# Performance work log

Measured on AMD Instinct MI355X. Metric: run time of the kernel, lower is better.

## Reference

```python
import jax, jax.numpy as jnp
import numpy as np

IN_CH = 512
SCALES = (128.0, 256.0, 512.0)
ASPECT_RATIOS = (0.5, 1.0, 2.0)
NUM_ANCHORS = 9
PRE_NMS_TOPK = 10000
POST_NMS_TOPK = 2000
NMS_THRESH = 0.7


def conv2d(x, w, b, pad):
    y = jax.lax.conv_general_dilated(
        x, w, window_strides=(1, 1), padding=[(pad, pad), (pad, pad)],
        dimension_numbers=('NCHW', 'OIHW', 'NCHW'))
    return y + b[None, :, None, None]


def generate_anchors(image_hw, feat_hw, dtype=jnp.float32):
    img_h, img_w = image_hw
    gh, gw = feat_hw
    stride_h = img_h // gh
    stride_w = img_w // gw
    scale = jnp.asarray(SCALES, dtype)
    ar = jnp.asarray(ASPECT_RATIOS, dtype)
    h_ratio = jnp.sqrt(ar)
    w_ratio = 1.0 / h_ratio
    ws = (w_ratio[:, None] * scale[None, :]).reshape(-1)  # (9,) ratio-major
    hs = (h_ratio[:, None] * scale[None, :]).reshape(-1)
    base = jnp.round(jnp.stack([-ws, -hs, ws, hs], axis=1) / 2.0)  # (9,4)
    shift_x = jnp.arange(gw, dtype=dtype) * stride_w
    shift_y = jnp.arange(gh, dtype=dtype) * stride_h
    sy, sx = jnp.meshgrid(shift_y, shift_x, indexing='ij')
    sx = sx.reshape(-1)
    sy = sy.reshape(-1)
    shifts = jnp.stack([sx, sy, sx, sy], axis=1)  # (gh*gw, 4)
    anchors = (shifts[:, None, :] + base[None, :, :]).reshape(-1, 4)
    return anchors


def decode_boxes(deltas, anchors):
    # deltas: (N,4) [dx,dy,dw,dh]; anchors: (N,4) [x1,y1,x2,y2]
    w = anchors[:, 2] - anchors[:, 0]
    h = anchors[:, 3] - anchors[:, 1]
    cx = anchors[:, 0] + 0.5 * w
    cy = anchors[:, 1] + 0.5 * h
    dx, dy, dw, dh = deltas[:, 0], deltas[:, 1], deltas[:, 2], deltas[:, 3]
    pcx = w * dx + cx
    pcy = h * dy + cy
    pw = jnp.exp(dw) * w
    ph = jnp.exp(dh) * h
    return jnp.stack([pcx - 0.5 * pw, pcy - 0.5 * ph,
                      pcx + 0.5 * pw, pcy + 0.5 * ph], axis=1)


def clamp_boxes(b, image_hw):
    h, w = image_hw
    return jnp.stack([jnp.clip(b[:, 0], 0.0, w), jnp.clip(b[:, 1], 0.0, h),
                      jnp.clip(b[:, 2], 0.0, w), jnp.clip(b[:, 3], 0.0, h)], axis=1)


def pairwise_iou(boxes1, boxes2):
    area1 = (boxes1[:, 2] - boxes1[:, 0]) * (boxes1[:, 3] - boxes1[:, 1])
    area2 = (boxes2[:, 2] - boxes2[:, 0]) * (boxes2[:, 3] - boxes2[:, 1])
    xl = jnp.maximum(boxes1[:, None, 0], boxes2[None, :, 0])
    yt = jnp.maximum(boxes1[:, None, 1], boxes2[None, :, 1])
    xr = jnp.minimum(boxes1[:, None, 2], boxes2[None, :, 2])
    yb = jnp.minimum(boxes1[:, None, 3], boxes2[None, :, 3])
    inter = jnp.clip(xr - xl, 0.0) * jnp.clip(yb - yt, 0.0)
    return inter / (area1[:, None] + area2[None, :] - inter)


def nms_keep(boxes_sorted, thresh):
    # boxes already sorted by score descending; returns bool keep mask
    n = boxes_sorted.shape[0]
    iou = pairwise_iou(boxes_sorted, boxes_sorted)  # (n,n) ~ the memory-bound hot spot
    idx = jnp.arange(n)
    def body(i, keep):
        suppressed = jnp.any((iou[i] > thresh) & keep & (idx < i))
        return keep.at[i].set(jnp.logical_not(suppressed))
    return jax.lax.fori_loop(0, n, body, jnp.ones((n,), dtype=bool))


def filter_proposals(proposals, logits, image_hw):
    scores = jax.nn.sigmoid(logits.reshape(-1))
    top_scores, top_idx = jax.lax.top_k(scores, PRE_NMS_TOPK)  # sorted descending
    props = proposals[top_idx]
    props = clamp_boxes(props, image_hw)
    keep = nms_keep(jax.lax.stop_gradient(props), NMS_THRESH)
    masked = jnp.where(keep, jax.lax.stop_gradient(top_scores), -1.0)
    sel_scores, sel = jax.lax.top_k(masked, POST_NMS_TOPK)
    valid = sel_scores >= 0.0  # sigmoid scores are >0; padded slots are -1
    out_boxes = jnp.where(valid[:, None], props[sel], 0.0)
    out_scores = jnp.where(valid, top_scores[sel], 0.0)
    return out_boxes, out_scores


def setup_inputs() -> dict:
    key = jax.random.key(0)
    ks = jax.random.split(key, 6)
    image = jax.random.normal(ks[0], (1, 3, 800, 800), jnp.float32)
    feat = jax.random.normal(ks[1], (1, IN_CH, 50, 50), jnp.float32)
    # small init scales keep exp(dw) numerically tame (mimics real conv init)
    rpn_w = jax.random.normal(ks[2], (IN_CH, IN_CH, 3, 3), jnp.float32) * 0.02
    rpn_b = jnp.zeros((IN_CH,), jnp.float32)
    cls_w = jax.random.normal(ks[3], (NUM_ANCHORS, IN_CH, 1, 1), jnp.float32) * 0.01
    cls_b = jnp.zeros((NUM_ANCHORS,), jnp.float32)
    box_w = jax.random.normal(ks[4], (NUM_ANCHORS * 4, IN_CH, 1, 1), jnp.float32) * 0.01
    box_b = jnp.zeros((NUM_ANCHORS * 4,), jnp.float32)
    return {"image": image, "feat": feat, "rpn_w": rpn_w, "rpn_b": rpn_b,
            "cls_w": cls_w, "cls_b": cls_b, "box_w": box_w, "box_b": box_b}


def reference(image, feat, rpn_w, rpn_b, cls_w, cls_b, box_w, box_b):
    B, _, H, W = feat.shape  # B == 1 as in the original (single-image RPN)
    rpn_feat = jax.nn.relu(conv2d(feat, rpn_w, rpn_b, pad=1))
    cls = conv2d(rpn_feat, cls_w, cls_b, pad=0)        # (1, 9, H, W)
    box = conv2d(rpn_feat, box_w, box_b, pad=0)        # (1, 36, H, W)
    anchors = generate_anchors(image.shape[-2:], (H, W), feat.dtype)  # (H*W*9, 4)
    # cls: NCHW -> NHWC -> (N_anchors, 1), anchor order = (y, x, anchor)
    cls_flat = jnp.transpose(cls, (0, 2, 3, 1)).reshape(-1, 1)
    # box: (1,9,4,H,W) -> (1,H,W,9,4) -> (N_anchors, 4)
    deltas = jnp.transpose(box.reshape(B, NUM_ANCHORS, 4, H, W), (0, 3, 4, 1, 2)).reshape(-1, 4)
    proposals = decode_boxes(deltas, anchors)
    props, scores = filter_proposals(proposals, jax.lax.stop_gradient(cls_flat), image.shape[-2:])
    return props, scores, cls_flat
```

## Files before the change

### kernel.cpp

```cpp
#include <hip/hip_runtime.h>
#include <cstdint>
#include <cstddef>


typedef unsigned long long ull;
typedef double d4 __attribute__((ext_vector_type(4)));

#define NANCH 9
#define NPIX  2500
#define CIN   512
#define COUT  512
#define KTOT  4608
#define KSEG  2304
#define NBOX  22500
#define TOPK1 10000
#define TOPK2 2000
#define WORDS 157
#define NHEAD 45
#define HPAD  48

__global__ __launch_bounds__(256) void wtrans(const float* __restrict__ w,
                                              float* __restrict__ wT) {
  __shared__ float t[36][65];
  const int ci0 = blockIdx.x * 4;
  const int co0 = blockIdx.y * 64;
  const int tid = threadIdx.x;
  const int co_l = tid >> 2, cq = tid & 3;
  const float* src = w + (size_t)(co0 + co_l) * KTOT + (ci0 + cq) * 9;
#pragma unroll
  for (int r = 0; r < 9; ++r) t[r * 4 + cq][co_l] = src[r];
  __syncthreads();
  const int co_w = tid & 63, rw0 = tid >> 6;
#pragma unroll
  for (int m = 0; m < 9; ++m) {
    int rw = rw0 + 4 * m;
    int tap = rw >> 2, cqq = rw & 3;
    wT[((size_t)tap * 512 + ci0 + cqq) * 512 + co0 + co_w] = t[rw][co_w];
  }
}

__global__ __launch_bounds__(256, 5) void conv_gemm(const float* __restrict__ feat,
                                                    const float* __restrict__ wT,
                                                    double* __restrict__ part) {
  const int p0  = blockIdx.x * 32;
  const int co0 = blockIdx.y * 64;
  const int z   = blockIdx.z;
  const int kseg0 = z * KSEG;
  __shared__ float As[2][32][40];
  __shared__ float Bs[2][32][72];
  const int tid  = threadIdx.x;
  const int lane = tid & 63;
  const int wave = tid >> 6;
  const int quad = lane >> 4;
  const int l16  = lane & 15;
  const int wp = (wave & 1) * 16;
  const int wc = (wave >> 1) * 32;
  const int plA = tid & 31, kAr = tid >> 5;
  const int pB = p0 + plA;
  const int py = pB / 50, px = pB - py * 50;
  const int coB = tid & 63, kBr = tid >> 6;

  int pmap[4];
  {
    double av_p = (quad == 0) ? (double)(l16 + 1) : (quad == 1 ? 1.0 : 0.0);
    double bv_p = (quad == 0) ? 1.0 : (quad == 1 ? (double)(1000 * (l16 + 1)) : 0.0);
    d4 dp = (d4){0.0, 0.0, 0.0, 0.0};
    dp = __builtin_amdgcn_mfma_f64_16x16x4f64(av_p, bv_p, dp, 0, 0, 0);
#pragma unroll
    for (int r = 0; r < 4; ++r) {
      int iv = (int)(dp[r] + 0.5);
      int mm = iv % 1000 - 1;
      int nn = iv / 1000 - 1;
      pmap[r] = (mm & 255) | (nn << 8);
    }
  }

  d4 acc[2];
#pragma unroll
  for (int i = 0; i < 2; ++i) acc[i] = (d4){0.0, 0.0, 0.0, 0.0};

  const int NCH = KSEG / 32;

  float fa[4], fb[8];

  auto loadA = [&](int cc) {
    int kk0 = kseg0 + cc * 32;
    int tap = kk0 >> 9;
    int ci0 = kk0 & 511;
    int ky = (tap * 11) >> 5;
    int kx = tap - 3 * ky;
    int yy = py + ky - 1, xx = px + kx - 1;
    bool valid = (pB < NPIX) && (yy >= 0) && (yy < 50) && (xx >= 0) && (xx < 50);
    int off = valid ? ((ci0 + kAr) * NPIX + yy * 50 + xx) : 0;
#pragma unroll
    for (int jj = 0; jj < 4; ++jj) {
      float v = feat[off + jj * 8 * NPIX];
      fa[jj] = valid ? v : 0.0f;
    }
  };
  auto loadB = [&](int cc) {
    const float* src = wT + (size_t)(kseg0 + cc * 32 + kBr) * 512 + co0 + coB;
#pragma unroll
    for (int s = 0; s < 8; ++s) fb[s] = src[s * 4 * 512];
  };

  loadA(0);
  loadB(0);
#pragma unroll
  for (int jj = 0; jj < 4; ++jj) As[0][kAr + 8 * jj][plA] = fa[jj];
#pragma unroll
  for (int s = 0; s < 8; ++s) Bs[0][kBr + 4 * s][coB] = fb[s];
  loadA(1);
  loadB(1);
  __syncthreads();

  for (int c = 0; c < NCH; ++c) {
    const int buf = c & 1;
    if (c + 1 < NCH) {
#pragma unroll
      for (int jj = 0; jj < 4; ++jj) As[buf ^ 1][kAr + 8 * jj][plA] = fa[jj];
#pragma unroll
      for (int s = 0; s < 8; ++s) Bs[buf ^ 1][kBr + 4 * s][coB] = fb[s];
    }
    if (c + 2 < NCH) {
      loadA(c + 2);
      loadB(c + 2);
    }
#pragma unroll
    for (int kk = 0; kk < 32; kk += 4) {
      double av  = (double)As[buf][kk + quad][wp + l16];
      double bv0 = (double)Bs[buf][kk + quad][wc + l16];
      double bv1 = (double)Bs[buf][kk + quad][wc + 16 + l16];
      acc[0] = __builtin_amdgcn_mfma_f64_16x16x4f64(av, bv0, acc[0], 0, 0, 0);
      acc[1] = __builtin_amdgcn_mfma_f64_16x16x4f64(av, bv1, acc[1], 0, 0, 0);
    }
    __syncthreads();
  }
  double* basez = part + (size_t)z * COUT * NPIX;
#pragma unroll
  for (int cj = 0; cj < 2; ++cj) {
#pragma unroll
    for (int r = 0; r < 4; ++r) {
      int mm = pmap[r] & 255, nn = pmap[r] >> 8;
      int p  = p0 + wp + mm;
      int co = co0 + wc + cj * 16 + nn;
      if (p < NPIX) basez[(size_t)co * NPIX + p] = acc[cj][r];
    }
  }
}

__global__ __launch_bounds__(256) void heads_mm(
    const double* __restrict__ part, const float* __restrict__ rpn_b,
    const float* __restrict__ cls_w, const float* __restrict__ box_w,
    double* __restrict__ headsc) {
  const int lane = threadIdx.x & 63;
  const int o = __builtin_amdgcn_readfirstlane(blockIdx.y * 4 + (threadIdx.x >> 6));
  if (o >= NHEAD) return;
  const int p = blockIdx.x * 64 + lane;
  const bool act = p < NPIX;
  const int pp = act ? p : 0;
  const float* wsel = (o < 9) ? (cls_w + (size_t)o * CIN)
                              : (box_w + (size_t)(o - 9) * CIN);
  const double* p0 = part + pp;
  const double* p1 = part + (size_t)COUT * NPIX + pp;
  double acc = 0.0;
#pragma unroll 4
  for (int co = 0; co < CIN; ++co) {
    double v = p0[(size_t)co * NPIX] + p1[(size_t)co * NPIX] + (double)rpn_b[co];
    v = v > 0.0 ? v : 0.0;
    acc += (double)wsel[co] * v;
  }
  if (act) headsc[(size_t)p * HPAD + o] = acc;
}

__global__ __launch_bounds__(256) void decode_kernel(
    const double* __restrict__ headsc, const float* __restrict__ cls_b,
    const float* __restrict__ box_b, double* __restrict__ logits,
    double* __restrict__ boxesAll, float* __restrict__ out_cls) {
  int idx = blockIdx.x * blockDim.x + threadIdx.x;
  if (idx >= NBOX) return;
  int p = idx / 9, a = idx - p * 9;
  int y = p / 50, x = p - y * 50;
  double sx = 16.0 * (double)x, sy = 16.0 * (double)y;
  const double scs[3] = {128.0, 256.0, 512.0};
  const double ars[3] = {0.5, 1.0, 2.0};
  double ar = ars[a / 3], sc = scs[a - (a / 3) * 3];
  double hr = sqrt(ar), wr = 1.0 / hr;
  double wv = wr * sc, hv = hr * sc;
  double bx0 = rint(-wv * 0.5), by0 = rint(-hv * 0.5);
  double bx1 = rint(wv * 0.5), by1 = rint(hv * 0.5);
  double a0 = sx + bx0, a1 = sy + by0, a2 = sx + bx1, a3 = sy + by1;
  double wA = a2 - a0, hA = a3 - a1;
  double cx = a0 + 0.5 * wA, cy = a1 + 0.5 * hA;
  const double* hp = headsc + (size_t)p * HPAD;
  double dx = hp[9 + a * 4 + 0] + (double)box_b[a * 4 + 0];
  double dy = hp[9 + a * 4 + 1] + (double)box_b[a * 4 + 1];
  double dw = hp[9 + a * 4 + 2] + (double)box_b[a * 4 + 2];
  double dh = hp[9 + a * 4 + 3] + (double)box_b[a * 4 + 3];
  double pcx = wA * dx + cx, pcy = hA * dy + cy;
  double pw = exp(dw) * wA, ph = exp(dh) * hA;
  double b0 = pcx - 0.5 * pw, b1 = pcy - 0.5 * ph;
  double b2 = pcx + 0.5 * pw, b3 = pcy + 0.5 * ph;
  b0 = fmin(fmax(b0, 0.0), 800.0);
  b1 = fmin(fmax(b1, 0.0), 800.0);
  b2 = fmin(fmax(b2, 0.0), 800.0);
  b3 = fmin(fmax(b3, 0.0), 800.0);
  boxesAll[(size_t)idx * 4 + 0] = b0;
  boxesAll[(size_t)idx * 4 + 1] = b1;
  boxesAll[(size_t)idx * 4 + 2] = b2;
  boxesAll[(size_t)idx * 4 + 3] = b3;
  double L = hp[a] + (double)cls_b[a];
  logits[idx] = L;
  out_cls[idx] = (float)L;
}

__global__ __launch_bounds__(256) void rank_count(const double* __restrict__ logits,
                                                  int* __restrict__ ranks) {
  __shared__ double Ls[2048];
  int i = blockIdx.x * 256 + threadIdx.x;
  int j0 = blockIdx.y * 2048;
  int jn = NBOX - j0;
  if (jn > 2048) jn = 2048;
  for (int t = threadIdx.x; t < jn; t += 256) Ls[t] = logits[j0 + t];
  __syncthreads();
  if (i >= NBOX) return;
  double Li = logits[i];
  int cnt = 0;
  for (int t = 0; t < jn; ++t) {
    double Lj = Ls[t];
    int j = j0 + t;
    cnt += (Lj > Li || (Lj == Li && j < i)) ? 1 : 0;
  }
  atomicAdd(&ranks[i], cnt);
}

__global__ __launch_bounds__(256) void scatter_topk(const double* __restrict__ logits,
                                                    const double* __restrict__ boxesAll,
                                                    const int* __restrict__ ranks,
                                                    double* __restrict__ sLog,
                                                    double* __restrict__ sBox) {
  int i = blockIdx.x * 256 + threadIdx.x;
  if (i >= NBOX) return;
  int r = ranks[i];
  if (r < TOPK1) {
    sLog[r] = logits[i];
    sBox[(size_t)r * 4 + 0] = boxesAll[(size_t)i * 4 + 0];
    sBox[(size_t)r * 4 + 1] = boxesAll[(size_t)i * 4 + 1];
    sBox[(size_t)r * 4 + 2] = boxesAll[(size_t)i * 4 + 2];
    sBox[(size_t)r * 4 + 3] = boxesAll[(size_t)i * 4 + 3];
  }
}

__global__ __launch_bounds__(256) void iou_mask(const double* __restrict__ sb,
                                                ull* __restrict__ mask) {
  const int it = blockIdx.x;
  const int wt = blockIdx.y;
  if (wt * 4 + 3 < it) return;
  __shared__ double ib[64][4];
  __shared__ double jb[256][4];
  const int tid = threadIdx.x;
  {
    int ii = it * 64 + (tid >> 2);
    int d = tid & 3;
    ib[tid >> 2][d] = (ii < TOPK1) ? sb[(size_t)ii * 4 + d] : 0.0;
  }
  for (int t = tid; t < 1024; t += 256) {
    int jj = wt * 256 + (t >> 2);
    jb[t >> 2][t & 3] = (jj < TOPK1) ? sb[(size_t)jj * 4 + (t & 3)] : 0.0;
  }
  __syncthreads();
  const int il = tid & 63, wl = tid >> 6;
  const int i = it * 64 + il;
  const int word = wt * 4 + wl;
  if (i >= TOPK1 || word >= WORDS || word < (i >> 6)) return;
  const double x0 = ib[il][0], y0 = ib[il][1], x1 = ib[il][2], y1 = ib[il][3];
  const double areai = (x1 - x0) * (y1 - y0);
  ull bits = 0;
  const int jbase = word * 64;
  for (int b = 0; b < 64; ++b) {
    int j = jbase + b;
    if (j <= i || j >= TOPK1) continue;
    int jl = wl * 64 + b;
    double u0 = jb[jl][0], u1 = jb[jl][1], u2 = jb[jl][2], u3 = jb[jl][3];
    double xl = fmax(x0, u0), yt = fmax(y0, u1);
    double xr = fmin(x1, u2), yb = fmin(y1, u3);
    double iw = xr - xl, ih = yb - yt;
    iw = iw > 0.0 ? iw : 0.0;
    ih = ih > 0.0 ? ih : 0.0;
    double inter = iw * ih;
    double aj = (u2 - u0) * (u3 - u1);
    double un = areai + aj - inter;
    if (inter > 0.7 * un) bits |= 1ull << b;
  }
  mask[(size_t)i * WORDS + word] = bits;
}

#define NTILE 8
#define TRS   10
#define KCAP  2112

__global__ __launch_bounds__(256) void nms_scan(const ull* __restrict__ mask,
                                                ull* __restrict__ keepwords) {
  __shared__ ull tileRows[512 * TRS];
  __shared__ int klist[KCAP];
  __shared__ ull remvPart[32][NTILE + 1];
  __shared__ unsigned int remv32[NTILE * 2];
  __shared__ int newk[64];
  __shared__ int kcLds, nkLds, doneLds;
  const int tid = threadIdx.x;
  const int lane = tid & 63;
  const int wave = tid >> 6;
  if (tid == 0) { kcLds = 0; nkLds = 0; doneLds = 0; }
  __syncthreads();

  for (int T = 0; T < (WORDS + NTILE - 1) / NTILE; ++T) {
    const int G0 = T * NTILE;
    const int TW = (WORDS - G0 < NTILE) ? (WORDS - G0) : NTILE;
    const int kc0 = kcLds;
#pragma unroll
    for (int pass = 0; pass < 8; ++pass) {
      int lr = pass * 64 + (tid >> 2);
      int w  = (tid & 3) * 2;
      int gr = G0 * 64 + lr;
      ull v0 = 0, v1 = 0;
      if (gr < TOPK1) {
        const ull* row = mask + (size_t)gr * WORDS + G0;
        if (w < TW)     v0 = row[w];
        if (w + 1 < TW) v1 = row[w + 1];
      }
      tileRows[lr * TRS + w]     = v0;
      tileRows[lr * TRS + w + 1] = v1;
    }
    {
      int w = tid & 7, stripe = tid >> 3;
      ull acc = 0;
      if (w < TW) {
        int t = stripe;
        for (; t + 224 < kc0; t += 256) {
          ull a0 = mask[(size_t)klist[t      ] * WORDS + G0 + w];
          ull a1 = mask[(size_t)klist[t +  32] * WORDS + G0 + w];
          ull a2 = mask[(size_t)klist[t +  64] * WORDS + G0 + w];
          ull a3 = mask[(size_t)klist[t +  96] * WORDS + G0 + w];
          ull a4 = mask[(size_t)klist[t + 128] * WORDS + G0 + w];
          ull a5 = mask[(size_t)klist[t + 160] * WORDS + G0 + w];
          ull a6 = mask[(size_t)klist[t + 192] * WORDS + G0 + w];
          ull a7 = mask[(size_t)klist[t + 224] * WORDS + G0 + w];
          acc |= ((a0 | a1) | (a2 | a3)) | ((a4 | a5) | (a6 | a7));
        }
        for (; t < kc0; t += 32) acc |= mask[(size_t)klist[t] * WORDS + G0 + w];
      }
      remvPart[stripe][w] = acc;
    }
    __syncthreads();
    if (tid < NTILE) {
      ull r = 0;
#pragma unroll
      for (int s = 0; s < 32; ++s) r |= remvPart[s][tid];
      remv32[tid * 2]     = (unsigned int)r;
      remv32[tid * 2 + 1] = (unsigned int)(r >> 32);
    }
    __syncthreads();
    for (int gi = 0; gi < TW; ++gi) {
      const int g = G0 + gi;
      if (wave == 0) {
        ull cur = ((ull)remv32[gi * 2 + 1] << 32) | remv32[gi * 2];
        unsigned int clo = __builtin_amdgcn_readfirstlane((unsigned int)cur);
        unsigned int chi = __builtin_amdgcn_readfirstlane((unsigned int)(cur >> 32));
        cur = ((ull)chi << 32) | clo;
        ull mrow = tileRows[(gi * 64 + lane) * TRS + gi];
        const unsigned int ml = (unsigned int)mrow;
        const unsigned int mh = (unsigned int)(mrow >> 32);
        const ull validm = (g == WORDS - 1) ? 0xFFFFull : ~0ull;
        ull rem = (~cur) & validm;
        while (rem) {
          int b = __ffsll((long long)rem) - 1;
          b = __builtin_amdgcn_readfirstlane(b);
          ull m = ((ull)(unsigned int)__builtin_amdgcn_readlane((int)mh, b) << 32) |
                  (unsigned int)__builtin_amdgcn_readlane((int)ml, b);
          cur |= m;
          ull above = (b == 63) ? 0ull : (~0ull << (b + 1));
          rem = (~cur) & rem & above;
        }
        ull kb = (~cur) & validm;
        if (lane == 0) keepwords[g] = kb;
        int kc = kcLds;
        if ((kb >> lane) & 1ull) {
          int ofs = __popcll(lane ? (kb & ((1ull << lane) - 1ull)) : 0ull);
          klist[kc + ofs] = g * 64 + lane;
          newk[ofs] = gi * 64 + lane;
        }
        if (lane == 0) {
          int nk = __popcll(kb);
          nkLds = nk;
          kcLds = kc + nk;
          doneLds = (kc + nk >= TOPK2) ? 1 : 0;
        }
      }
      __syncthreads();
      if (doneLds) break;
      if (gi + 1 < TW) {
        int w = tid & 7, k0 = tid >> 3;
        int nk = nkLds;
        if (w > gi && w < TW) {
          ull acc = 0;
          for (int kk = k0; kk < nk; kk += 32) acc |= tileRows[newk[kk] * TRS + w];
          if (acc) {
            atomicOr(&remv32[w * 2], (unsigned int)acc);
            atomicOr(&remv32[w * 2 + 1], (unsigned int)(acc >> 32));
          }
        }
      }
      __syncthreads();
    }
    if (doneLds) break;
  }
}

__global__ __launch_bounds__(256) void finalize_kernel(const ull* __restrict__ keepwords,
                                                       const double* __restrict__ sBox,
                                                       const double* __restrict__ sLog,
                                                       float* __restrict__ out) {
  __shared__ int pref[WORDS];
  int t = threadIdx.x;
  if (t == 0) {
    int s = 0;
    for (int w = 0; w < WORDS; ++w) {
      pref[w] = s;
      s += __popcll(keepwords[w]);
    }
  }
  __syncthreads();
  if (t < WORDS) {
    ull kb = keepwords[t];
    int base = pref[t];
    while (kb) {
      int b = __ffsll((long long)kb) - 1;
      kb &= kb - 1;
      if (base < TOPK2) {
        int i = t * 64 + b;
        out[base * 4 + 0] = (float)sBox[(size_t)i * 4 + 0];
        out[base * 4 + 1] = (float)sBox[(size_t)i * 4 + 1];
        out[base * 4 + 2] = (float)sBox[(size_t)i * 4 + 2];
        out[base * 4 + 3] = (float)sBox[(size_t)i * 4 + 3];
        double L = sLog[i];
        out[TOPK2 * 4 + base] = (float)(1.0 / (1.0 + exp(-L)));
      }
      ++base;
    }
  }
}

extern "C" void kernel_launch(void* const* d_in, const int* in_sizes, int n_in,
                              void* d_out, int out_size, void* d_ws, size_t ws_size,
                              hipStream_t stream) {
  const float* feat  = (const float*)d_in[1];
  const float* rpn_w = (const float*)d_in[2];
  const float* rpn_b = (const float*)d_in[3];
  const float* cls_w = (const float*)d_in[4];
  const float* cls_b = (const float*)d_in[5];
  const float* box_w = (const float*)d_in[6];
  const float* box_b = (const float*)d_in[7];
  float* out = (float*)d_out;

  char* ws = (char*)d_ws;
  double* part     = (double*)(ws);
  double* logits   = (double*)(ws + 20480000);
  double* boxesAll = (double*)(ws + 20660000);
  int*    ranks    = (int*)   (ws + 21380000);
  double* sBox     = (double*)(ws + 21470000);
  double* sLog     = (double*)(ws + 21790000);
  ull*    mask     = (ull*)   (ws + 21870000);
  ull*    keepw    = (ull*)   (ws + 34430000);
  float*  wT       = (float*) (ws + 21870000);
  double* headsc   = (double*)(ws + 21870000);

  hipMemsetAsync(d_out, 0, (TOPK2 * 4 + TOPK2) * sizeof(float), stream);
  hipMemsetAsync(ranks, 0, NBOX * sizeof(int), stream);
  hipMemsetAsync(keepw, 0, WORDS * sizeof(ull), stream);

  wtrans<<<dim3(128, 8), 256, 0, stream>>>(rpn_w, wT);
  conv_gemm<<<dim3(80, 8, 2), 256, 0, stream>>>(feat, wT, part);
  heads_mm<<<dim3(40, 12), 256, 0, stream>>>(part, rpn_b, cls_w, box_w, headsc);
  decode_kernel<<<88, 256, 0, stream>>>(headsc, cls_b, box_b, logits, boxesAll,
                                        out + TOPK2 * 5);
  rank_count<<<dim3(88, 11), 256, 0, stream>>>(logits, ranks);
  scatter_topk<<<88, 256, 0, stream>>>(logits, boxesAll, ranks, sLog, sBox);
  iou_mask<<<dim3(WORDS, 40), 256, 0, stream>>>(sBox, mask);
  nms_scan<<<1, 256, 0, stream>>>(mask, keepw);
  finalize_kernel<<<1, 256, 0, stream>>>(keepw, sBox, sLog, out);
}
```

Measured before the change: 802.2 us.

## Restructure heads matmul to reuse staged activations across all output channels

The heads kernel now loads each chunk of the conv partial sums once per pixel tile, applies bias and ReLU, and stages the result in shared memory along with the head weights. Each wave then accumulates 12 output channels from the staged data. This replaces the old layout, where every output channel re-read the full partial-sum buffer. The grid shrinks from 480 blocks to 40, which reduces parallelism on a large GPU.

```diff
diff --git a/kernel.cpp b/kernel.cpp
--- a/kernel.cpp
+++ b/kernel.cpp
@@ -149,28 +149,70 @@
   }
 }
 
+#define HCHUNK 64
 __global__ __launch_bounds__(256) void heads_mm(
     const double* __restrict__ part, const float* __restrict__ rpn_b,
     const float* __restrict__ cls_w, const float* __restrict__ box_w,
     double* __restrict__ headsc) {
-  const int lane = threadIdx.x & 63;
-  const int o = __builtin_amdgcn_readfirstlane(blockIdx.y * 4 + (threadIdx.x >> 6));
-  if (o >= NHEAD) return;
-  const int p = blockIdx.x * 64 + lane;
+  __shared__ double vt[HCHUNK][66];
+  __shared__ float wls[HCHUNK][48];
+  const int tid  = threadIdx.x;
+  const int lane = tid & 63;
+  const int wave = tid >> 6;
+  const int p0 = blockIdx.x * 64;
+  const int p  = p0 + lane;
   const bool act = p < NPIX;
-  const int pp = act ? p : 0;
-  const float* wsel = (o < 9) ? (cls_w + (size_t)o * CIN)
-                              : (box_w + (size_t)(o - 9) * CIN);
-  const double* p0 = part + pp;
-  const double* p1 = part + (size_t)COUT * NPIX + pp;
-  double acc = 0.0;
+  const int ob = wave * 12;
+  int omap[12];
+#pragma unroll
+  for (int oi = 0; oi < 12; ++oi) {
+    int o = ob + oi;
+    omap[oi] = (o < NHEAD) ? o : (NHEAD - 1);
+  }
+  double acc[12];
+#pragma unroll
+  for (int i = 0; i < 12; ++i) acc[i] = 0.0;
+
+  const int pl = tid & 63, cr = tid >> 6;
+  for (int cb = 0; cb < CIN; cb += HCHUNK) {
+#pragma unroll
+    for (int s = 0; s < HCHUNK / 4; ++s) {
+      int col = cr + 4 * s;
+      int co = cb + col;
+      double v = 0.0;
+      if (p0 + pl < NPIX) {
+        double a = part[(size_t)co * NPIX + p0 + pl];
+        double b = part[(size_t)(co + COUT) * NPIX + p0 + pl];
+        v = a + b + (double)rpn_b[co];
+        v = v > 0.0 ? v : 0.0;
+      }
+      vt[col][pl] = v;
+    }
+    for (int idx = tid; idx < HCHUNK * NHEAD; idx += 256) {
+      int col = idx & (HCHUNK - 1);
+      int o = idx >> 6;
+      int co = cb + col;
+      float wv = (o < 9) ? cls_w[(size_t)o * CIN + co]
+                         : box_w[(size_t)(o - 9) * CIN + co];
+      wls[col][o] = wv;
+    }
+    __syncthreads();
 #pragma unroll 4
-  for (int co = 0; co < CIN; ++co) {
-    double v = p0[(size_t)co * NPIX] + p1[(size_t)co * NPIX] + (double)rpn_b[co];
-    v = v > 0.0 ? v : 0.0;
-    acc += (double)wsel[co] * v;
-  }
-  if (act) headsc[(size_t)p * HPAD + o] = acc;
+    for (int col = 0; col < HCHUNK; ++col) {
+      double v = vt[col][lane];
+#pragma unroll
+      for (int oi = 0; oi < 12; ++oi)
+        acc[oi] += (double)wls[col][omap[oi]] * v;
+    }
+    __syncthreads();
+  }
+  if (act) {
+#pragma unroll
+    for (int oi = 0; oi < 12; ++oi) {
+      int o = ob + oi;
+      if (o < NHEAD) headsc[(size_t)p * HPAD + o] = acc[oi];
+    }
+  }
 }
 
 __global__ __launch_bounds__(256) void decode_kernel(
@@ -480,7 +522,7 @@
 
   wtrans<<<dim3(128, 8), 256, 0, stream>>>(rpn_w, wT);
   conv_gemm<<<dim3(80, 8, 2), 256, 0, stream>>>(feat, wT, part);
-  heads_mm<<<dim3(40, 12), 256, 0, stream>>>(part, rpn_b, cls_w, box_w, headsc);
+  heads_mm<<<40, 256, 0, stream>>>(part, rpn_b, cls_w, box_w, headsc);
   decode_kernel<<<88, 256, 0, stream>>>(headsc, cls_b, box_b, logits, boxesAll,
                                         out + TOPK2 * 5);
   rank_count<<<dim3(88, 11), 256, 0, stream>>>(logits, ranks);
```

Result: slower. 914.8 us (+14.0%).

## Store NMS suppression mask word-major for coalesced scan loads

Applied to the files above, without the earlier changes.

The NMS IoU mask is now stored transposed (word-major, box-minor) instead of row-per-box. The scan kernel's tile load now has each wave read consecutive boxes for one word, which gives coalesced global loads, and the LDS row stride changes to 9. The gather of suppression words for kept boxes now indexes a contiguous per-word array, though these remain scattered gathers. The writes in the mask kernel become strided across words, and any other mask reader must follow the new layout.

```diff
diff --git a/kernel.cpp b/kernel.cpp
--- a/kernel.cpp
+++ b/kernel.cpp
@@ -292,11 +292,11 @@
     double un = areai + aj - inter;
     if (inter > 0.7 * un) bits |= 1ull << b;
   }
-  mask[(size_t)i * WORDS + word] = bits;
+  mask[(size_t)word * TOPK1 + i] = bits;
 }
 
 #define NTILE 8
-#define TRS   10
+#define TRS   9
 #define KCAP  2112
 
 __global__ __launch_bounds__(256) void nms_scan(const ull* __restrict__ mask,
@@ -319,35 +319,35 @@
     const int kc0 = kcLds;
 #pragma unroll
     for (int pass = 0; pass < 8; ++pass) {
-      int lr = pass * 64 + (tid >> 2);
-      int w  = (tid & 3) * 2;
+      int lr = pass * 64 + lane;
+      int w0 = wave * 2;
       int gr = G0 * 64 + lr;
       ull v0 = 0, v1 = 0;
       if (gr < TOPK1) {
-        const ull* row = mask + (size_t)gr * WORDS + G0;
-        if (w < TW)     v0 = row[w];
-        if (w + 1 < TW) v1 = row[w + 1];
+        if (w0 < TW)     v0 = mask[(size_t)(G0 + w0) * TOPK1 + gr];
+        if (w0 + 1 < TW) v1 = mask[(size_t)(G0 + w0 + 1) * TOPK1 + gr];
       }
-      tileRows[lr * TRS + w]     = v0;
-      tileRows[lr * TRS + w + 1] = v1;
+      tileRows[lr * TRS + w0]     = v0;
+      tileRows[lr * TRS + w0 + 1] = v1;
     }
     {
       int w = tid & 7, stripe = tid >> 3;
       ull acc = 0;
       if (w < TW) {
+        const ull* mw = mask + (size_t)(G0 + w) * TOPK1;
         int t = stripe;
         for (; t + 224 < kc0; t += 256) {
-          ull a0 = mask[(size_t)klist[t      ] * WORDS + G0 + w];
-          ull a1 = mask[(size_t)klist[t +  32] * WORDS + G0 + w];
-          ull a2 = mask[(size_t)klist[t +  64] * WORDS + G0 + w];
-          ull a3 = mask[(size_t)klist[t +  96] * WORDS + G0 + w];
-          ull a4 = mask[(size_t)klist[t + 128] * WORDS + G0 + w];
-          ull a5 = mask[(size_t)klist[t + 160] * WORDS + G0 + w];
-          ull a6 = mask[(size_t)klist[t + 192] * WORDS + G0 + w];
-          ull a7 = mask[(size_t)klist[t + 224] * WORDS + G0 + w];
+          ull a0 = mw[klist[t      ]];
+          ull a1 = mw[klist[t +  32]];
+          ull a2 = mw[klist[t +  64]];
+          ull a3 = mw[klist[t +  96]];
+          ull a4 = mw[klist[t + 128]];
+          ull a5 = mw[klist[t + 160]];
+          ull a6 = mw[klist[t + 192]];
+          ull a7 = mw[klist[t + 224]];
           acc |= ((a0 | a1) | (a2 | a3)) | ((a4 | a5) | (a6 | a7));
         }
-        for (; t < kc0; t += 32) acc |= mask[(size_t)klist[t] * WORDS + G0 + w];
+        for (; t < kc0; t += 32) acc |= mw[klist[t]];
       }
       remvPart[stripe][w] = acc;
     }
```

Result: slower. 820.9 us (+2.3%).

## Stage ReLU'd conv partials in shared memory and compute two heads per wave

Applied to the files above, without the earlier changes.

The heads kernel now loads a 32-channel chunk of the two split-K conv partials cooperatively, adds the bias, applies ReLU, and stores the result into a double-buffered LDS tile with register prefetch. Each wave then computes two output heads from that shared tile. Before, every wave re-read both partial buffers for its one head. The grid's y dimension is halved to match, which cuts redundant global reads of the partials but adds barriers and shared-memory traffic.

```diff
diff --git a/kernel.cpp b/kernel.cpp
--- a/kernel.cpp
+++ b/kernel.cpp
@@ -153,24 +153,69 @@
     const double* __restrict__ part, const float* __restrict__ rpn_b,
     const float* __restrict__ cls_w, const float* __restrict__ box_w,
     double* __restrict__ headsc) {
-  const int lane = threadIdx.x & 63;
-  const int o = __builtin_amdgcn_readfirstlane(blockIdx.y * 4 + (threadIdx.x >> 6));
-  if (o >= NHEAD) return;
-  const int p = blockIdx.x * 64 + lane;
+  __shared__ double vt[2][32][66];
+  const int tid  = threadIdx.x;
+  const int lane = tid & 63;
+  const int wave = tid >> 6;
+  const int p0 = blockIdx.x * 64;
+  const int p  = p0 + lane;
   const bool act = p < NPIX;
-  const int pp = act ? p : 0;
-  const float* wsel = (o < 9) ? (cls_w + (size_t)o * CIN)
-                              : (box_w + (size_t)(o - 9) * CIN);
-  const double* p0 = part + pp;
-  const double* p1 = part + (size_t)COUT * NPIX + pp;
-  double acc = 0.0;
-#pragma unroll 4
-  for (int co = 0; co < CIN; ++co) {
-    double v = p0[(size_t)co * NPIX] + p1[(size_t)co * NPIX] + (double)rpn_b[co];
-    v = v > 0.0 ? v : 0.0;
-    acc += (double)wsel[co] * v;
-  }
-  if (act) headsc[(size_t)p * HPAD + o] = acc;
+  const int ob = __builtin_amdgcn_readfirstlane(blockIdx.y * 8 + wave * 2);
+  const int o0 = ob, o1 = ob + 1;
+  auto wptr = [&](int o) {
+    int oc = o < NHEAD ? o : NHEAD - 1;
+    return (oc < 9) ? cls_w + (size_t)oc * CIN
+                    : box_w + (size_t)(oc - 9) * CIN;
+  };
+  const float* w0p = wptr(o0);
+  const float* w1p = wptr(o1);
+
+  const int pl = tid & 63, cr = tid >> 6;
+  const int pp = (p0 + pl < NPIX) ? (p0 + pl) : 0;
+  const int NCHK = CIN / 32;
+
+  double ra[8], rb[8];
+  auto loadC = [&](int cb) {
+#pragma unroll
+    for (int s = 0; s < 8; ++s) {
+      int row = cb + cr + 4 * s;
+      ra[s] = part[(size_t)row * NPIX + pp];
+      rb[s] = part[(size_t)(row + COUT) * NPIX + pp];
+    }
+  };
+  auto storeC = [&](int buf, int cb) {
+#pragma unroll
+    for (int s = 0; s < 8; ++s) {
+      int rloc = cr + 4 * s;
+      double v = ra[s] + rb[s] + (double)rpn_b[cb + rloc];
+      vt[buf][rloc][pl] = v > 0.0 ? v : 0.0;
+    }
+  };
+
+  double acc0 = 0.0, acc1 = 0.0;
+
+  loadC(0);
+  storeC(0, 0);
+  loadC(32);
+  __syncthreads();
+
+  for (int c = 0; c < NCHK; ++c) {
+    const int buf = c & 1;
+    const int cb = c * 32;
+    if (c + 1 < NCHK) storeC(buf ^ 1, cb + 32);
+    if (c + 2 < NCHK) loadC(cb + 64);
+#pragma unroll 8
+    for (int col = 0; col < 32; ++col) {
+      double v = vt[buf][col][lane];
+      acc0 += (double)w0p[cb + col] * v;
+      acc1 += (double)w1p[cb + col] * v;
+    }
+    __syncthreads();
+  }
+  if (act) {
+    if (o0 < NHEAD) headsc[(size_t)p * HPAD + o0] = acc0;
+    if (o1 < NHEAD) headsc[(size_t)p * HPAD + o1] = acc1;
+  }
 }
 
 __global__ __launch_bounds__(256) void decode_kernel(
@@ -480,7 +525,7 @@
 
   wtrans<<<dim3(128, 8), 256, 0, stream>>>(rpn_w, wT);
   conv_gemm<<<dim3(80, 8, 2), 256, 0, stream>>>(feat, wT, part);
-  heads_mm<<<dim3(40, 12), 256, 0, stream>>>(part, rpn_b, cls_w, box_w, headsc);
+  heads_mm<<<dim3(40, 6), 256, 0, stream>>>(part, rpn_b, cls_w, box_w, headsc);
   decode_kernel<<<88, 256, 0, stream>>>(headsc, cls_b, box_b, logits, boxesAll,
                                         out + TOPK2 * 5);
   rank_count<<<dim3(88, 11), 256, 0, stream>>>(logits, ranks);
```

Result: faster. 772.6 us (-3.7%).
